# Performance work log

Hardware: AMD Instinct MI355X
Metric: run time of the kernel (lower is better)

The kernel has to match this reference:

```python
import jax, jax.numpy as jnp
import numpy as np

# ---- static config (from module code / init_kwargs) ----
D_MODEL = 512
D_STATE = 64
D_CONV = 4
EXPAND = 2
HEADDIM = 64
D_INNER = EXPAND * D_MODEL          # 1024
NHEADS = D_INNER // HEADDIM         # 16
D_IN_PROJ = 2 * D_INNER + 2 * D_STATE + NHEADS  # 2192
CONV_DIM = D_INNER + 2 * D_STATE    # 1152
N_LAYERS = 2
VOCAB = 32768
BATCH = 2
SEQ = 512
EPS = 1e-5


def setup_inputs() -> dict:
    key = jax.random.key(0)
    ks = jax.random.split(key, 12)
    g = lambda k, shape, s=0.02: (jax.random.normal(k, shape, jnp.float32) * s)
    return {
        "input_ids": jax.random.randint(ks[0], (BATCH, SEQ), 0, VOCAB),
        "padding_mask": jnp.zeros((BATCH, SEQ), dtype=bool),  # True = pad
        "embeddings": g(ks[1], (VOCAB, D_MODEL)),
        "in_proj_w": g(ks[2], (N_LAYERS, D_IN_PROJ, D_MODEL)),
        "conv_w": g(ks[3], (N_LAYERS, CONV_DIM, D_CONV), 0.1),
        "conv_b": jnp.zeros((N_LAYERS, CONV_DIM), jnp.float32),
        "dt_bias": g(ks[4], (N_LAYERS, NHEADS), 0.5),
        "A_log": jnp.log(jax.random.uniform(ks[5], (N_LAYERS, NHEADS), jnp.float32, 1.0, 16.0)),
        "D_ssm": jnp.ones((N_LAYERS, NHEADS), jnp.float32),
        "norm_w": jnp.ones((N_LAYERS, D_INNER), jnp.float32),
        "out_proj_w": g(ks[6], (N_LAYERS, D_MODEL, D_INNER)),
        "aggr_w": g(ks[7], (D_MODEL, 2 * D_MODEL)),
        "aggr_b": jnp.zeros((D_MODEL,), jnp.float32),
        "norm_f_w": jnp.ones((D_MODEL,), jnp.float32),
        "lm_head_w": g(ks[8], (VOCAB, D_MODEL)),
        "lm_head_b": jnp.zeros((VOCAB,), jnp.float32),
    }


def rmsnorm(x, w):
    return x * jax.lax.rsqrt(jnp.mean(x * x, axis=-1, keepdims=True) + EPS) * w


def flip_sc(X, padding_mask):
    # reverse the valid (non-pad) prefix of each sequence, leave pad positions in place
    b, l, _ = X.shape
    lengths = jnp.sum(~padding_mask, axis=1)                        # (b,)
    pos = jnp.arange(l)[None, :]                                    # (1,l)
    keep = pos < lengths[:, None]
    rev = jnp.where(keep, lengths[:, None] - 1 - pos, pos)          # (b,l)
    return jnp.take_along_axis(X, rev[:, :, None], axis=1)


def causal_conv(x, w, b):
    # x: (b,l,c); depthwise causal conv with kernel size D_CONV
    xt = jnp.transpose(x, (0, 2, 1))                                # (b,c,l)
    y = jax.lax.conv_general_dilated(
        xt, w[:, None, :], window_strides=(1,), padding=[(D_CONV - 1, 0)],
        feature_group_count=w.shape[0], dimension_numbers=("NCH", "OIH", "NCH"))
    return jnp.transpose(y + b[None, :, None], (0, 2, 1))


def ssd_scan(x, dt, A, B, C):
    # x:(b,l,h,p) dt:(b,l,h) A:(h,) B,C:(b,l,n) -> y:(b,l,h,p)
    bsz = x.shape[0]
    dA = jnp.exp(dt * A)                                            # (b,l,h)
    dtx = dt[..., None] * x                                         # (b,l,h,p)
    def step(h, inp):
        dA_t, dtx_t, B_t, C_t = inp
        h = h * dA_t[:, :, None, None] + dtx_t[..., None] * B_t[:, None, None, :]
        y = jnp.einsum("bhpn,bn->bhp", h, C_t)
        return h, y
    h0 = jnp.zeros((bsz, NHEADS, HEADDIM, D_STATE), x.dtype)
    xs = (jnp.swapaxes(dA, 0, 1), jnp.swapaxes(dtx, 0, 1),
          jnp.swapaxes(B, 0, 1), jnp.swapaxes(C, 0, 1))
    _, ys = jax.lax.scan(step, h0, xs)
    return jnp.swapaxes(ys, 0, 1)


def mamba2_block(x, wi, cw, cb, dtb, alog, dss, nw, wo):
    # Mamba2 layer with residual (EncoderLayer: mamba(X) + X)
    b, l, _ = x.shape
    zxbcdt = jnp.einsum("bld,ed->ble", x, wi)                      # (b,l,D_IN_PROJ)
    z = zxbcdt[..., :D_INNER]
    xBC = zxbcdt[..., D_INNER:D_INNER + CONV_DIM]
    dt = jax.nn.softplus(zxbcdt[..., D_INNER + CONV_DIM:] + dtb)   # (b,l,h)
    xBC = jax.nn.silu(causal_conv(xBC, cw, cb))
    xs = xBC[..., :D_INNER].reshape(b, l, NHEADS, HEADDIM)
    B = xBC[..., D_INNER:D_INNER + D_STATE]
    C = xBC[..., D_INNER + D_STATE:]
    A = -jnp.exp(alog)                                             # (h,)
    y = ssd_scan(xs, dt, A, B, C) + xs * dss[None, None, :, None]
    y = y.reshape(b, l, D_INNER)
    y = rmsnorm(y * jax.nn.silu(z), nw)                            # RMSNormGated
    return jnp.einsum("ble,de->bld", y, wo) + x


def reference(input_ids, padding_mask, embeddings, in_proj_w, conv_w, conv_b,
              dt_bias, A_log, D_ssm, norm_w, out_proj_w, aggr_w, aggr_b,
              norm_f_w, lm_head_w, lm_head_b):
    X = embeddings[input_ids]                                      # (b,l,d)
    for i in range(N_LAYERS):
        X_flip = flip_sc(X, padding_mask)
        X_f = mamba2_block(X, in_proj_w[i], conv_w[i], conv_b[i], dt_bias[i],
                           A_log[i], D_ssm[i], norm_w[i], out_proj_w[i])
        X_b = mamba2_block(X_flip, in_proj_w[i], conv_w[i], conv_b[i], dt_bias[i],
                           A_log[i], D_ssm[i], norm_w[i], out_proj_w[i])
        X_b = flip_sc(X_b, padding_mask)
        # gated bidirectional fusion
        zg = jax.nn.sigmoid(jnp.concatenate([X_f, X_b], axis=-1) @ aggr_w.T + aggr_b)
        X = zg * X_f + (1.0 - zg) * X_b
    h = rmsnorm(X, norm_f_w)
    logits = h @ lm_head_w.T + lm_head_b                            # (b,l,V)
    return logits
```

## Files before the change

### kernel.cpp

```cpp
#include <hip/hip_runtime.h>

#define SEQ    512
#define DM     512
#define DI     1024
#define NH     16
#define DS     64
#define CONVD  1152
#define DPROJ  2192
#define NPADIN 2304

typedef __attribute__((ext_vector_type(8))) short bf16x8;
typedef __attribute__((ext_vector_type(4))) float floatx4;

__device__ __forceinline__ unsigned int f2bf(float f) {
  unsigned int u = __float_as_uint(f);
  u += 0x7FFFu + ((u >> 16) & 1u);
  return u >> 16;
}
__device__ __forceinline__ ushort4 cvt4(float4 v) {
  ushort4 o;
  o.x = (unsigned short)f2bf(v.x); o.y = (unsigned short)f2bf(v.y);
  o.z = (unsigned short)f2bf(v.z); o.w = (unsigned short)f2bf(v.w);
  return o;
}
__device__ __forceinline__ float sigmoidf_(float x) { return 1.f / (1.f + __expf(-x)); }
__device__ __forceinline__ float siluf_(float x) { return x * sigmoidf_(x); }

__device__ __forceinline__ void gl16(const void* g, void* l) {
  __builtin_amdgcn_global_load_lds(
      (const __attribute__((address_space(1))) unsigned int*)g,
      (__attribute__((address_space(3))) unsigned int*)l, 16, 0, 0);
}

template<int BM, int BN, int EPI>
__global__ __launch_bounds__(256) void gemm_bf(
    const short* __restrict__ A, const short* __restrict__ B,
    float* __restrict__ C, const int K, const int Nvalid, const int ldc,
    const float* __restrict__ e0, const float* __restrict__ e1,
    unsigned short* __restrict__ o2)
{
  constexpr int FM = BM / 32, FN = BN / 32;
  constexpr int PA = BM / 32, PB = BN / 32;
  __shared__ short As[BM * 64];
  __shared__ short Bs[BN * 64];
  const int tid = threadIdx.x, lane = tid & 63, wave = tid >> 6;
  const int m0 = blockIdx.y * BM, n0 = blockIdx.x * BN;
  const int wm = (wave >> 1) * (BM / 2), wn = (wave & 1) * (BN / 2);
  const int prow = wave * 8 + (lane >> 3);
  const int schk = ((lane & 7) ^ (prow & 7)) << 3;
  const short* agp = A + (size_t)(m0 + prow) * K + schk;
  const short* bgp = B + (size_t)(n0 + prow) * K + schk;
  short* albase = &As[wave * 8 * 64];
  short* blbase = &Bs[wave * 8 * 64];
  const int r16 = lane & 15, quad = lane >> 4;

  floatx4 acc[FM][FN];
#pragma unroll
  for (int i = 0; i < FM; i++)
#pragma unroll
    for (int j = 0; j < FN; j++) acc[i][j] = (floatx4)0.f;

  for (int k0 = 0; k0 < K; k0 += 64) {
#pragma unroll
    for (int p = 0; p < PA; ++p)
      gl16(agp + (size_t)p * 32 * K + k0, albase + p * 32 * 64);
#pragma unroll
    for (int p = 0; p < PB; ++p)
      gl16(bgp + (size_t)p * 32 * K + k0, blbase + p * 32 * 64);
    __syncthreads();
#pragma unroll
    for (int kk = 0; kk < 2; ++kk) {
      bf16x8 afr[FM], bfr[FN];
#pragma unroll
      for (int i = 0; i < FM; i++) {
        const int row = wm + i * 16 + r16;
        afr[i] = *(const bf16x8*)&As[row * 64 + (((kk * 4 + quad) ^ (row & 7)) << 3)];
      }
#pragma unroll
      for (int j = 0; j < FN; j++) {
        const int row = wn + j * 16 + r16;
        bfr[j] = *(const bf16x8*)&Bs[row * 64 + (((kk * 4 + quad) ^ (row & 7)) << 3)];
      }
#pragma unroll
      for (int i = 0; i < FM; i++)
#pragma unroll
        for (int j = 0; j < FN; j++)
          acc[i][j] = __builtin_amdgcn_mfma_f32_16x16x32_bf16(afr[i], bfr[j], acc[i][j], 0, 0, 0);
    }
    __syncthreads();
  }

  const int er = quad << 2;
#pragma unroll
  for (int i = 0; i < FM; ++i)
#pragma unroll
    for (int j = 0; j < FN; ++j)
#pragma unroll
      for (int r = 0; r < 4; ++r) {
        const int gm = m0 + wm + i * 16 + er + r;
        const int gn = n0 + wn + j * 16 + r16;
        float v = acc[i][j][r];
        if (EPI == 0) {
          if (gn < Nvalid) C[(size_t)gm * ldc + gn] = v;
        } else if (EPI == 1) {
          const int mm = gm & 1023;
          v += e0[(size_t)mm * DM + gn];
          const size_t idx = (size_t)mm * DI + ((gm >> 10) << 9) + gn;
          C[idx] = v;
          o2[idx] = (unsigned short)f2bf(v);
        } else if (EPI == 2) {
          const float zg = sigmoidf_(v + e0[gn]);
          const float xn = zg * e1[(size_t)gm * DI + gn] +
                           (1.f - zg) * e1[(size_t)gm * DI + DM + gn];
          const size_t idx = (size_t)gm * DM + gn;
          C[idx] = xn;
          o2[idx] = (unsigned short)f2bf(xn);
        } else {
          C[(size_t)gm * ldc + gn] = v + e0[gn];
        }
      }
}

#define WO4  262144
#define AW4  131072
#define LM4  4194304
__global__ __launch_bounds__(256) void prep_k(
    const int* __restrict__ ids, const float* __restrict__ emb,
    const float* __restrict__ wi, const float* __restrict__ wo,
    const float* __restrict__ aw, const float* __restrict__ lmw,
    float* __restrict__ Xf, unsigned short* __restrict__ Xb,
    unsigned short* __restrict__ wiB, unsigned short* __restrict__ woB,
    unsigned short* __restrict__ awB, unsigned short* __restrict__ lmwB) {
  const int blk = blockIdx.x, tid = threadIdx.x;
  if (blk < 512) {
    const int m = blk * 2 + (tid >> 7), col = tid & 127;
    const int row = ids[m];
    float4 v = ((const float4*)(emb + (size_t)row * DM))[col];
    ((float4*)(Xf + (size_t)m * DM))[col] = v;
    ((ushort4*)(Xb + (size_t)m * DM))[col] = cvt4(v);
  } else if (blk < 512 + 2304) {
    const int slot = (blk - 512) * 2 + (tid >> 7), col = tid & 127;
    const int l = slot >= 2304 ? 1 : 0;
    const int row = slot - l * 2304;
    ushort4 o; o.x = o.y = o.z = o.w = 0;
    if (row < DPROJ)
      o = cvt4(((const float4*)(wi + ((size_t)l * DPROJ + row) * DM))[col]);
    ((ushort4*)(wiB + ((size_t)l * NPADIN + row) * DM))[col] = o;
  } else {
    for (int i = (blk - 2816) * 256 + tid; i < WO4 + AW4 + LM4; i += 4480 * 256) {
      int j = i;
      const float4* s; ushort4* d;
      if (j < WO4)            { s = (const float4*)wo;  d = (ushort4*)woB; }
      else if (j < WO4 + AW4) { j -= WO4; s = (const float4*)aw;  d = (ushort4*)awB; }
      else                    { j -= WO4 + AW4; s = (const float4*)lmw; d = (ushort4*)lmwB; }
      d[j] = cvt4(s[j]);
    }
  }
}

__global__ __launch_bounds__(256) void conv_k(const float* __restrict__ zx,
    const float* __restrict__ cw, const float* __restrict__ cb,
    const float* __restrict__ dtb, const float* __restrict__ alog,
    float* __restrict__ xact, float* __restrict__ dtt, float* __restrict__ dAt) {
  const int t0 = (blockIdx.x & 31) << 4;
  const int half = blockIdx.x >> 5;
  const int b = blockIdx.y;
  const float* src = zx + (size_t)b * SEQ * DPROJ + DI;
  float* d0 = xact + (size_t)b * SEQ * CONVD;
  float* d1 = xact + (size_t)(2 + b) * SEQ * CONVD;

  for (int cc = 0; cc < 3; ++cc) {
    const int ci = cc * 256 + threadIdx.x;
    if (ci >= 576) break;
    const int c = half * 576 + ci;
    const float w0 = cw[c*4+0], w1 = cw[c*4+1], w2 = cw[c*4+2], w3 = cw[c*4+3];
    const float bias = cb[c];
    float a_[22];
#pragma unroll
    for (int j = 0; j < 22; ++j) {
      const int t = t0 - 3 + j;
      a_[j] = (t >= 0 && t < SEQ) ? src[(size_t)t * DPROJ + c] : 0.f;
    }
#pragma unroll
    for (int tt = 0; tt < 16; ++tt) {
      const float f = bias + w0*a_[tt]   + w1*a_[tt+1] + w2*a_[tt+2] + w3*a_[tt+3];
      const float g = bias + w3*a_[tt+3] + w2*a_[tt+4] + w1*a_[tt+5] + w0*a_[tt+6];
      d0[(size_t)(t0+tt) * CONVD + c] = siluf_(f);
      d1[(size_t)(t0+tt) * CONVD + c] = siluf_(g);
    }
  }
  if (half == 0) {
    const int hh = threadIdx.x >> 4, tt2 = threadIdx.x & 15;
    const int t = t0 + tt2;
    const float v = zx[(size_t)(b * SEQ + t) * DPROJ + 2176 + hh] + dtb[hh];
    const float dt = (v > 15.f) ? v : log1pf(__expf(v));
    const float A = -__expf(alog[hh]);
    dtt[(b * NH + hh) * SEQ + t] = dt;
    dAt[(b * NH + hh) * SEQ + t] = __expf(dt * A);
  }
}

__global__ __launch_bounds__(256, 1) void scan_k(const float* __restrict__ xact,
    const float* __restrict__ dtt, const float* __restrict__ dAt,
    float* __restrict__ yn) {
  const int bid = blockIdx.x;
  const int dir = bid >> 7, b = (bid >> 6) & 1, h = (bid >> 2) & 15;
  const int ph = (bid >> 1) & 1, nh = bid & 1;
  const int tid = threadIdx.x, lane = tid & 63, wave = tid >> 6;
  const int pl = tid & 31, nq = tid >> 5;
  const int nb = nq << 2;
  const float* __restrict__ src = xact + (size_t)(dir * 2 + b) * SEQ * CONVD;
  const float* __restrict__ dtp = dtt + (b * NH + h) * SEQ;
  const float* __restrict__ dap = dAt + (b * NH + h) * SEQ;
  float* __restrict__ yrow = yn + (size_t)nh * (4 * SEQ * DI)
      + (size_t)(dir * 2 + b) * SEQ * DI + h * 64 + ph * 32;

  __shared__ __align__(16) float sdt[SEQ];
  __shared__ __align__(16) float sda[SEQ];
  __shared__ __align__(16) float sBC[2][16 * 64];
  __shared__ __align__(16) float sXV[2][16 * 32];
  __shared__ float yp[2][8][16][33];

  if (tid < 128)       ((float4*)sdt)[tid]       = ((const float4*)dtp)[tid];
  else                 ((float4*)sda)[tid - 128] = ((const float4*)dap)[tid - 128];

#define SCAN_STAGE(c0n, bufi) do {                                            \
    const int s_bc  = wave * 4 + (lane >> 4);                                 \
    const int half_ = (lane >> 3) & 1;                                        \
    const int part_ = lane & 7;                                               \
    const int tnb   = dir ? (SEQ - 1 - ((c0n) + s_bc)) : ((c0n) + s_bc);      \
    gl16(src + (size_t)tnb * CONVD + DI + half_ * DS + nh * 32 + part_ * 4,   \
         &sBC[bufi][wave * 256]);                                             \
    if (wave < 2) {                                                           \
      const int s_xv = wave * 8 + (lane >> 3);                                \
      const int tnx  = dir ? (SEQ - 1 - ((c0n) + s_xv)) : ((c0n) + s_xv);     \
      gl16(src + (size_t)tnx * CONVD + h * 64 + ph * 32 + part_ * 4,          \
           &sXV[bufi][wave * 256]);                                           \
    }                                                                         \
  } while (0)

  SCAN_STAGE(0, 0);
  __syncthreads();

  float hs[4] = {0.f, 0.f, 0.f, 0.f};
  int pb = 0, buf = 0;

  for (int c0 = 0; c0 < SEQ; c0 += 16, pb ^= 1, buf ^= 1) {
    if (c0 + 16 < SEQ) SCAN_STAGE(c0 + 16, buf ^ 1);
#pragma unroll
    for (int s = 0; s < 16; ++s) {
      const int tn = dir ? (SEQ - 1 - (c0 + s)) : (c0 + s);
      const float dts = sdt[tn];
      const float das = sda[tn];
      const float xv = sXV[buf][s * 32 + pl];
      const float4 b4 = *(const float4*)&sBC[buf][s * 64 + nb];
      const float4 c4 = *(const float4*)&sBC[buf][s * 64 + 32 + nb];
      const float dtx = dts * xv;
      float ya;
      hs[0] = hs[0] * das + dtx * b4.x; ya  = hs[0] * c4.x;
      hs[1] = hs[1] * das + dtx * b4.y; ya += hs[1] * c4.y;
      hs[2] = hs[2] * das + dtx * b4.z; ya += hs[2] * c4.z;
      hs[3] = hs[3] * das + dtx * b4.w; ya += hs[3] * c4.w;
      yp[pb][nq][s][pl] = ya;
    }
    __syncthreads();
    {
      const int rt = tid >> 4, rp = (tid & 15) << 1;
      const int tn = dir ? (SEQ - 1 - (c0 + rt)) : (c0 + rt);
      float s0 = 0.f, s1 = 0.f;
#pragma unroll
      for (int j = 0; j < 8; ++j) { s0 += yp[pb][j][rt][rp]; s1 += yp[pb][j][rt][rp + 1]; }
      float2 o; o.x = s0; o.y = s1;
      *(float2*)&yrow[(size_t)tn * DI + rp] = o;
    }
  }
#undef SCAN_STAGE
}

__global__ __launch_bounds__(256) void p2_k(const float* __restrict__ yn,
    const float* __restrict__ xact, const float* __restrict__ zx,
    const float* __restrict__ dss, const float* __restrict__ nw,
    unsigned short* __restrict__ A2b) {
  const int m2 = blockIdx.x;
  const int e4 = threadIdx.x << 2;
  const float4 ya = *(const float4*)(yn + (size_t)m2 * DI + e4);
  const float4 yb = *(const float4*)(yn + (size_t)4 * SEQ * DI + (size_t)m2 * DI + e4);
  const float4 x4 = *(const float4*)(xact + (size_t)m2 * CONVD + e4);
  const float4 z4 = *(const float4*)(zx + (size_t)(m2 & 1023) * DPROJ + e4);
  const float d = dss[e4 >> 6];
  float4 g;
  g.x = (ya.x + yb.x + x4.x * d) * siluf_(z4.x);
  g.y = (ya.y + yb.y + x4.y * d) * siluf_(z4.y);
  g.z = (ya.z + yb.z + x4.z * d) * siluf_(z4.z);
  g.w = (ya.w + yb.w + x4.w * d) * siluf_(z4.w);
  float ss = g.x*g.x + g.y*g.y + g.z*g.z + g.w*g.w;
#pragma unroll
  for (int m = 32; m >= 1; m >>= 1) ss += __shfl_xor(ss, m);
  __shared__ float red[4];
  if ((threadIdx.x & 63) == 0) red[threadIdx.x >> 6] = ss;
  __syncthreads();
  const float tot = red[0] + red[1] + red[2] + red[3];
  const float sc = rsqrtf(tot * (1.f / 1024.f) + 1e-5f);
  const float4 w4 = *(const float4*)(nw + e4);
  float4 o;
  o.x = g.x * sc * w4.x; o.y = g.y * sc * w4.y;
  o.z = g.z * sc * w4.z; o.w = g.w * sc * w4.w;
  ((ushort4*)(A2b + (size_t)m2 * DI))[threadIdx.x] = cvt4(o);
}

__global__ __launch_bounds__(128) void fnorm_k(const float* __restrict__ X,
    const float* __restrict__ w, unsigned short* __restrict__ outb) {
  const int m = blockIdx.x;
  const int e4 = threadIdx.x << 2;
  const float4 x4 = *(const float4*)(X + (size_t)m * DM + e4);
  float ss = x4.x*x4.x + x4.y*x4.y + x4.z*x4.z + x4.w*x4.w;
#pragma unroll
  for (int mm = 32; mm >= 1; mm >>= 1) ss += __shfl_xor(ss, mm);
  __shared__ float red[2];
  if ((threadIdx.x & 63) == 0) red[threadIdx.x >> 6] = ss;
  __syncthreads();
  const float tot = red[0] + red[1];
  const float sc = rsqrtf(tot * (1.f / 512.f) + 1e-5f);
  const float4 w4 = *(const float4*)(w + e4);
  float4 o;
  o.x = x4.x * sc * w4.x; o.y = x4.y * sc * w4.y;
  o.z = x4.z * sc * w4.z; o.w = x4.w * sc * w4.w;
  ((ushort4*)(outb + (size_t)m * DM))[threadIdx.x] = cvt4(o);
}

extern "C" void kernel_launch(void* const* d_in, const int* in_sizes, int n_in,
                              void* d_out, int out_size, void* d_ws, size_t ws_size,
                              hipStream_t stream) {
  (void)in_sizes; (void)n_in; (void)out_size; (void)ws_size;
  const int*   ids  = (const int*)d_in[0];
  const float* emb  = (const float*)d_in[2];
  const float* wi   = (const float*)d_in[3];
  const float* cw   = (const float*)d_in[4];
  const float* cb   = (const float*)d_in[5];
  const float* dtb  = (const float*)d_in[6];
  const float* alog = (const float*)d_in[7];
  const float* dss  = (const float*)d_in[8];
  const float* nw   = (const float*)d_in[9];
  const float* wo   = (const float*)d_in[10];
  const float* aw   = (const float*)d_in[11];
  const float* ab   = (const float*)d_in[12];
  const float* nfw  = (const float*)d_in[13];
  const float* lmw  = (const float*)d_in[14];
  const float* lmb  = (const float*)d_in[15];
  float* out = (float*)d_out;

  float* ws    = (float*)d_ws;
  float* Xf    = ws;
  float* zx    = Xf    + (size_t)524288;
  float* xact  = zx    + (size_t)2244608;
  float* dtt   = xact  + (size_t)2359296;
  float* dAt   = dtt   + (size_t)16384;
  float* yn    = dAt   + (size_t)16384;
  float* Xcatf = yn    + (size_t)4194304;
  unsigned short* Xb    = (unsigned short*)(Xcatf + (size_t)1048576);
  unsigned short* A2b   = Xb    + (size_t)524288;
  unsigned short* Xcatb = A2b   + (size_t)2097152;
  unsigned short* hnb   = Xcatb + (size_t)1048576;
  unsigned short* wiB   = hnb   + (size_t)524288;
  unsigned short* woB   = wiB   + (size_t)2359296;
  unsigned short* awB   = woB   + (size_t)1048576;
  unsigned short* lmwB  = awB   + (size_t)524288;

  prep_k<<<dim3(7296), dim3(256), 0, stream>>>(ids, emb, wi, wo, aw, lmw,
                                               Xf, Xb, wiB, woB, awB, lmwB);

  for (int layer = 0; layer < 2; ++layer) {
    gemm_bf<128, 128, 0><<<dim3(18, 8), dim3(256), 0, stream>>>(
        (const short*)Xb, (const short*)(wiB + (size_t)layer * NPADIN * DM),
        zx, 512, 2192, 2192, nullptr, nullptr, nullptr);
    conv_k<<<dim3(64, 2), dim3(256), 0, stream>>>(
        zx, cw + (size_t)layer * 4608, cb + (size_t)layer * 1152,
        dtb + 16 * layer, alog + 16 * layer, xact, dtt, dAt);
    scan_k<<<dim3(256), dim3(256), 0, stream>>>(xact, dtt, dAt, yn);
    p2_k<<<dim3(2048), dim3(256), 0, stream>>>(yn, xact, zx, dss + 16 * layer,
                                               nw + (size_t)layer * 1024, A2b);
    gemm_bf<64, 128, 1><<<dim3(4, 32), dim3(256), 0, stream>>>(
        (const short*)A2b, (const short*)(woB + (size_t)layer * DM * DI),
        Xcatf, 1024, 512, 512, Xf, nullptr, Xcatb);
    gemm_bf<64, 64, 2><<<dim3(8, 16), dim3(256), 0, stream>>>(
        (const short*)Xcatb, (const short*)awB,
        Xf, 1024, 512, 512, ab, Xcatf, Xb);
  }
  fnorm_k<<<dim3(1024), dim3(128), 0, stream>>>(Xf, nfw, hnb);
  gemm_bf<128, 128, 3><<<dim3(256, 8), dim3(256), 0, stream>>>(
      (const short*)hnb, (const short*)lmwB, out, 512, 32768, 32768, lmb, nullptr, nullptr);
}
```

Measured before the change: 507.7 us.

## Split scan into more blocks with fewer states per thread and pre-reversed dt

Each scan block now covers 16 head-dim channels instead of 32 and each thread carries 2 state elements instead of 4. This doubles the grid to 512 blocks and lets two blocks share a CU, which shortens the serial recurrence chain per block. The dt/dA arrays are stored in shared memory already reversed for the backward direction so they can be loaded as vectors per chunk. The cross-thread reduction grows from 8 to 16 partial sums per output, and B/C rows are reloaded by twice as many blocks.

Result: no change. 508.2 us (+0.1%).

```diff
diff --git a/kernel.cpp b/kernel.cpp
--- a/kernel.cpp
+++ b/kernel.cpp
@@ -200,78 +200,82 @@
   }
 }
 
-__global__ __launch_bounds__(256, 1) void scan_k(const float* __restrict__ xact,
+__global__ __launch_bounds__(256, 2) void scan_k(const float* __restrict__ xact,
     const float* __restrict__ dtt, const float* __restrict__ dAt,
     float* __restrict__ yn) {
   const int bid = blockIdx.x;
-  const int dir = bid >> 7, b = (bid >> 6) & 1, h = (bid >> 2) & 15;
-  const int ph = (bid >> 1) & 1, nh = bid & 1;
+  const int dir = bid >> 8, b = (bid >> 7) & 1, h = (bid >> 3) & 15;
+  const int ph = (bid >> 1) & 3, nh = bid & 1;
   const int tid = threadIdx.x, lane = tid & 63, wave = tid >> 6;
-  const int pl = tid & 31, nq = tid >> 5;
-  const int nb = nq << 2;
+  const int pl = tid & 15, nq = tid >> 4;
+  const int nb = nq << 1;
   const float* __restrict__ src = xact + (size_t)(dir * 2 + b) * SEQ * CONVD;
   const float* __restrict__ dtp = dtt + (b * NH + h) * SEQ;
   const float* __restrict__ dap = dAt + (b * NH + h) * SEQ;
   float* __restrict__ yrow = yn + (size_t)nh * (4 * SEQ * DI)
-      + (size_t)(dir * 2 + b) * SEQ * DI + h * 64 + ph * 32;
+      + (size_t)(dir * 2 + b) * SEQ * DI + h * 64 + ph * 16;
 
   __shared__ __align__(16) float sdt[SEQ];
   __shared__ __align__(16) float sda[SEQ];
   __shared__ __align__(16) float sBC[2][16 * 64];
-  __shared__ __align__(16) float sXV[2][16 * 32];
-  __shared__ float yp[2][8][16][33];
-
-  if (tid < 128)       ((float4*)sdt)[tid]       = ((const float4*)dtp)[tid];
-  else                 ((float4*)sda)[tid - 128] = ((const float4*)dap)[tid - 128];
+  __shared__ __align__(16) float sXV[2][16 * 16];
+  __shared__ float yp[2][16][16][17];
+
+  {
+    const int i = tid * 2;
+    const int s0i = dir ? (SEQ - 1 - i) : i;
+    const int s1i = dir ? (SEQ - 2 - i) : (i + 1);
+    sdt[i]     = dtp[s0i];  sda[i]     = dap[s0i];
+    sdt[i + 1] = dtp[s1i];  sda[i + 1] = dap[s1i];
+  }
 
 #define SCAN_STAGE(c0n, bufi) do {                                            \
-    const int s_bc  = wave * 4 + (lane >> 4);                                 \
-    const int half_ = (lane >> 3) & 1;                                        \
-    const int part_ = lane & 7;                                               \
-    const int tnb   = dir ? (SEQ - 1 - ((c0n) + s_bc)) : ((c0n) + s_bc);      \
-    gl16(src + (size_t)tnb * CONVD + DI + half_ * DS + nh * 32 + part_ * 4,   \
+    const int sb  = wave * 4 + (lane >> 4);                                   \
+    const int idx = (lane & 15) * 4;                                          \
+    const int tnb = dir ? (SEQ - 1 - ((c0n) + sb)) : ((c0n) + sb);            \
+    gl16(src + (size_t)tnb * CONVD + DI + nh * 32 + idx + ((idx & 32) ? 32 : 0), \
          &sBC[bufi][wave * 256]);                                             \
-    if (wave < 2) {                                                           \
-      const int s_xv = wave * 8 + (lane >> 3);                                \
-      const int tnx  = dir ? (SEQ - 1 - ((c0n) + s_xv)) : ((c0n) + s_xv);     \
-      gl16(src + (size_t)tnx * CONVD + h * 64 + ph * 32 + part_ * 4,          \
-           &sXV[bufi][wave * 256]);                                           \
+    if (wave == 0) {                                                          \
+      const int sx  = lane >> 2;                                              \
+      const int tnx = dir ? (SEQ - 1 - ((c0n) + sx)) : ((c0n) + sx);          \
+      gl16(src + (size_t)tnx * CONVD + h * 64 + ph * 16 + (lane & 3) * 4,     \
+           &sXV[bufi][0]);                                                    \
     }                                                                         \
   } while (0)
 
   SCAN_STAGE(0, 0);
   __syncthreads();
 
-  float hs[4] = {0.f, 0.f, 0.f, 0.f};
+  float hs0 = 0.f, hs1 = 0.f;
   int pb = 0, buf = 0;
 
   for (int c0 = 0; c0 < SEQ; c0 += 16, pb ^= 1, buf ^= 1) {
     if (c0 + 16 < SEQ) SCAN_STAGE(c0 + 16, buf ^ 1);
+    float dtv[16], dav[16];
+#pragma unroll
+    for (int k = 0; k < 4; ++k) {
+      *(float4*)&dtv[k * 4] = ((const float4*)(sdt + c0))[k];
+      *(float4*)&dav[k * 4] = ((const float4*)(sda + c0))[k];
+    }
 #pragma unroll
     for (int s = 0; s < 16; ++s) {
-      const int tn = dir ? (SEQ - 1 - (c0 + s)) : (c0 + s);
-      const float dts = sdt[tn];
-      const float das = sda[tn];
-      const float xv = sXV[buf][s * 32 + pl];
-      const float4 b4 = *(const float4*)&sBC[buf][s * 64 + nb];
-      const float4 c4 = *(const float4*)&sBC[buf][s * 64 + 32 + nb];
-      const float dtx = dts * xv;
+      const float xv = sXV[buf][s * 16 + pl];
+      const float2 b2 = *(const float2*)&sBC[buf][s * 64 + nb];
+      const float2 c2 = *(const float2*)&sBC[buf][s * 64 + 32 + nb];
+      const float dtx = dtv[s] * xv;
       float ya;
-      hs[0] = hs[0] * das + dtx * b4.x; ya  = hs[0] * c4.x;
-      hs[1] = hs[1] * das + dtx * b4.y; ya += hs[1] * c4.y;
-      hs[2] = hs[2] * das + dtx * b4.z; ya += hs[2] * c4.z;
-      hs[3] = hs[3] * das + dtx * b4.w; ya += hs[3] * c4.w;
+      hs0 = hs0 * dav[s] + dtx * b2.x; ya  = hs0 * c2.x;
+      hs1 = hs1 * dav[s] + dtx * b2.y; ya += hs1 * c2.y;
       yp[pb][nq][s][pl] = ya;
     }
     __syncthreads();
     {
-      const int rt = tid >> 4, rp = (tid & 15) << 1;
+      const int rt = tid >> 4, rp = tid & 15;
       const int tn = dir ? (SEQ - 1 - (c0 + rt)) : (c0 + rt);
-      float s0 = 0.f, s1 = 0.f;
-#pragma unroll
-      for (int j = 0; j < 8; ++j) { s0 += yp[pb][j][rt][rp]; s1 += yp[pb][j][rt][rp + 1]; }
-      float2 o; o.x = s0; o.y = s1;
-      *(float2*)&yrow[(size_t)tn * DI + rp] = o;
+      float s0 = 0.f;
+#pragma unroll
+      for (int j = 0; j < 16; ++j) s0 += yp[pb][j][rt][rp];
+      yrow[(size_t)tn * DI + rp] = s0;
     }
   }
 #undef SCAN_STAGE
@@ -376,7 +380,7 @@
     conv_k<<<dim3(64, 2), dim3(256), 0, stream>>>(
         zx, cw + (size_t)layer * 4608, cb + (size_t)layer * 1152,
         dtb + 16 * layer, alog + 16 * layer, xact, dtt, dAt);
-    scan_k<<<dim3(256), dim3(256), 0, stream>>>(xact, dtt, dAt, yn);
+    scan_k<<<dim3(512), dim3(256), 0, stream>>>(xact, dtt, dAt, yn);
     p2_k<<<dim3(2048), dim3(256), 0, stream>>>(yn, xact, zx, dss + 16 * layer,
                                                nw + (size_t)layer * 1024, A2b);
     gemm_bf<64, 128, 1><<<dim3(4, 32), dim3(256), 0, stream>>>(
```
